# Performance work log

Hardware: AMD Instinct MI355X
Metric: run time of the kernel (lower is better)

## Reference

```python
import jax, jax.numpy as jnp
import numpy as np

FEATURES = 4096
BATCH = 2048


def setup_inputs() -> dict:
    key = jax.random.key(0)
    kx, kk = jax.random.split(key)
    x = jax.random.normal(kx, (BATCH, FEATURES), dtype=jnp.float32)
    kernel = jax.random.normal(kk, (FEATURES,), dtype=jnp.float32)
    return {"x": x, "kernel": kernel}


def reference(x, kernel):
    n = kernel.shape[0]
    i = jnp.arange(n)[:, None]   # [n,1]
    j = jnp.arange(n)[None, :]   # [1,n]
    idx = i - j                   # Toeplitz offsets
    # W[i,j] = kernel[i-j] if i>=j else 0  (causal lower-triangular Toeplitz)
    W = jnp.where(idx >= 0, kernel[jnp.clip(idx, 0, n - 1)], 0.0)
    # out[b,i] = sum_{j<=i} x[b,j] * kernel[i-j]  == x @ W.T
    return x @ W.T
```

## Files before the change

kernel.cpp:

```cpp
#include <hip/hip_runtime.h>
#include <hip/hip_bf16.h>


typedef unsigned short u16;
typedef __attribute__((ext_vector_type(8))) short  bf16x8;
typedef __attribute__((ext_vector_type(8))) unsigned short u16x8;
typedef __attribute__((ext_vector_type(4))) float  f32x4;

#define KDIM 4096
#define NDIM 4096
#define MDIM 2048
#define KREV_STRIDE 4608
#define KREV_BYTES  (8 * KREV_STRIDE * 2)
#define BSTRIDE 520

static __device__ inline u16 f2bf(float f) {
  unsigned u = __builtin_bit_cast(unsigned, f);
  unsigned r = u + 0x7FFFu + ((u >> 16) & 1u);
  return (u16)(r >> 16);
}

static __device__ inline void async_copy16(const void* g, void* l) {
  __builtin_amdgcn_global_load_lds((const __attribute__((address_space(1))) void*)g,
                                   (__attribute__((address_space(3))) void*)l,
                                   16, 0, 0);
}

__global__ __launch_bounds__(256) void prep(const float* __restrict__ x,
                                            const float* __restrict__ kern,
                                            u16* __restrict__ xb,
                                            u16* __restrict__ krevs,
                                            int conv_blocks) {
  int kb = (int)blockIdx.x - conv_blocks;
  if (kb >= 0) {
    int u = kb * 256 + threadIdx.x;
    for (int a = 0; a < 8; ++a) {
      int t = u + a - 8;
      u16 v = 0;
      if (t >= 0 && t <= 4095) v = f2bf(kern[4095 - t]);
      krevs[a * KREV_STRIDE + u] = v;
    }
  } else {
    size_t i = ((size_t)blockIdx.x * 256 + threadIdx.x) * 8;
    const f32x4* p = (const f32x4*)(x + i);
    f32x4 v0 = p[0], v1 = p[1];
    u16x8 r;
    r[0] = f2bf(v0[0]); r[1] = f2bf(v0[1]); r[2] = f2bf(v0[2]); r[3] = f2bf(v0[3]);
    r[4] = f2bf(v1[0]); r[5] = f2bf(v1[1]); r[6] = f2bf(v1[2]); r[7] = f2bf(v1[3]);
    *(u16x8*)(xb + i) = r;
  }
}

template <bool CONV>
__global__ __launch_bounds__(256, 3) void toeplitz_gemm(const void* __restrict__ Av,
                                                        const u16* __restrict__ krevs,
                                                        float* __restrict__ out) {
  __shared__ u16 A_lds[2][128 * 64];
  __shared__ u16 B_lds[2][8 * BSTRIDE];

  const int tid  = threadIdx.x;
  const int w    = tid >> 6;
  const int lane = tid & 63;
  const int lane16 = lane & 15;
  const int quad   = lane >> 4;
  const int wm = w >> 1;
  const int wn = w & 1;

  const int b    = (int)blockIdx.x;
  const int rank = (b < 256) ? b : 511 - (b & 255);
  const int ct   = 31 - (rank >> 4);
  const int n0   = ct * 128;
  const int m0   = (rank & 15) * 128;
  const int W    = 3968 - n0;

  int boff[4];
  for (int fn = 0; fn < 4; ++fn) {
    int n_g = n0 + wn * 64 + fn * 16 + lane16;
    int s0  = 4095 - n_g + quad * 8;
    int a   = s0 & 7;
    int ub  = s0 - a + 8 - W;
    boff[fn] = a * BSTRIDE + ub;
  }

  f32x4 acc[4][4] = {};
  const int nk = 2 * ct + 2;

  const int srow8 = lane >> 3;
  const int ssrc  = ((lane & 7) ^ srow8) * 8;

  const u16* xb = (const u16*)Av;
  const float* xf = (const float*)Av;

  auto stageA = [&](int ks) {
    const int buf = ks & 1;
    const int k0  = ks * 64;
    if constexpr (CONV) {
      int row  = tid & 127;
      int colq = tid >> 7;
      for (int lc = 0; lc < 4; ++lc) {
        int l = colq * 4 + lc;
        int p = l ^ (row & 7);
        const f32x4* px = (const f32x4*)(xf + (size_t)(m0 + row) * KDIM + k0 + l * 8);
        f32x4 v0 = px[0], v1 = px[1];
        u16x8 r;
        r[0]=f2bf(v0[0]); r[1]=f2bf(v0[1]); r[2]=f2bf(v0[2]); r[3]=f2bf(v0[3]);
        r[4]=f2bf(v1[0]); r[5]=f2bf(v1[1]); r[6]=f2bf(v1[2]); r[7]=f2bf(v1[3]);
        *(u16x8*)(&A_lds[buf][row * 64 + p * 8]) = r;
      }
    } else {
      for (int c = 0; c < 4; ++c) {
        int g   = c * 4 + w;
        int row = g * 8 + srow8;
        async_copy16(xb + (size_t)(m0 + row) * KDIM + k0 + ssrc,
                     &A_lds[buf][g * 512]);
      }
    }
  };
  auto stageB = [&](int ch) {
    const int bb = ch & 1;
    for (int cc = 0; cc < 2; ++cc) {
      int c = cc * 4 + w;
      async_copy16(krevs + c * KREV_STRIDE + W + ch * 256 + (lane << 3),
                   &B_lds[bb][c * BSTRIDE]);
    }
  };

  stageB(0);
  stageA(0);

  for (int ks = 0; ks < nk; ++ks) {
    __syncthreads();
    const int nxt = ks + 1;
    if (nxt < nk) {
      stageA(nxt);
      if ((nxt & 3) == 0) stageB(nxt >> 2);
    }
    const u16* Ab = A_lds[ks & 1];
    const u16* Bb = B_lds[(ks >> 2) & 1];
    const int ksl = (ks & 3) * 64;
    for (int kk = 0; kk < 2; ++kk) {
      bf16x8 af[4];
      const int p = (kk * 4 + quad) ^ (lane16 & 7);
      for (int fm = 0; fm < 4; ++fm) {
        int row = wm * 64 + fm * 16 + lane16;
        af[fm] = *(const bf16x8*)(&Ab[row * 64 + p * 8]);
      }
      bf16x8 bf[4];
      for (int fn = 0; fn < 4; ++fn)
        bf[fn] = *(const bf16x8*)(&Bb[boff[fn] + ksl + kk * 32]);
      for (int fm = 0; fm < 4; ++fm)
        for (int fn = 0; fn < 4; ++fn)
          acc[fm][fn] = __builtin_amdgcn_mfma_f32_16x16x32_bf16(af[fm], bf[fn], acc[fm][fn], 0, 0, 0);
    }
  }

  for (int fm = 0; fm < 4; ++fm) {
    int row_base = m0 + wm * 64 + fm * 16 + quad * 4;
    for (int fn = 0; fn < 4; ++fn) {
      int col = n0 + wn * 64 + fn * 16 + lane16;
      for (int r = 0; r < 4; ++r)
        out[(size_t)(row_base + r) * NDIM + col] = acc[fm][fn][r];
    }
  }
}

extern "C" void kernel_launch(void* const* d_in, const int* in_sizes, int n_in,
                              void* d_out, int out_size, void* d_ws, size_t ws_size,
                              hipStream_t stream) {
  const float* x    = (const float*)d_in[0];
  const float* kern = (const float*)d_in[1];
  float* out = (float*)d_out;

  u16* krevs = (u16*)d_ws;
  u16* xb    = (u16*)((char*)d_ws + KREV_BYTES);
  const size_t need_fast = (size_t)KREV_BYTES + (size_t)MDIM * KDIM * 2;

  if (ws_size >= need_fast) {
    prep<<<4096 + 18, 256, 0, stream>>>(x, kern, xb, krevs, 4096);
    toeplitz_gemm<false><<<512, 256, 0, stream>>>(xb, krevs, out);
  } else {
    prep<<<18, 256, 0, stream>>>(x, kern, xb, krevs, 0);
    toeplitz_gemm<true><<<512, 256, 0, stream>>>(x, krevs, out);
  }
}
```

Before: 135.9 us.

## Split K across two wave groups per block with LDS reduction

Doubles the block to 512 threads and splits each 128-wide K step between two groups of four waves. Each group accumulates its own half, and the partials are combined through shared memory before group 0 writes the output. Double buffering of A is replaced by one buffer per group, with two barriers per iteration. The goal is more waves in flight per tile to hide latency. The cost is extra synchronisation, more register pressure at 512 threads, and the reduction epilogue.

New measurement: 125.9 us. 7.3% less time.

```diff
diff --git a/kernel.cpp b/kernel.cpp
--- a/kernel.cpp
+++ b/kernel.cpp
@@ -52,19 +52,23 @@
 }
 
 template <bool CONV>
-__global__ __launch_bounds__(256, 3) void toeplitz_gemm(const void* __restrict__ Av,
+__global__ __launch_bounds__(512, 4) void toeplitz_gemm(const void* __restrict__ Av,
                                                         const u16* __restrict__ krevs,
                                                         float* __restrict__ out) {
-  __shared__ u16 A_lds[2][128 * 64];
-  __shared__ u16 B_lds[2][8 * BSTRIDE];
+  __shared__ __align__(16) char smem_raw[49408];
+  u16*   A_all = (u16*)smem_raw;
+  u16*   B_all = (u16*)(smem_raw + 32768);
+  f32x4* ep    = (f32x4*)smem_raw;
 
   const int tid  = threadIdx.x;
   const int w    = tid >> 6;
+  const int g    = w >> 2;
+  const int wl   = w & 3;
   const int lane = tid & 63;
   const int lane16 = lane & 15;
   const int quad   = lane >> 4;
-  const int wm = w >> 1;
-  const int wn = w & 1;
+  const int wm = wl >> 1;
+  const int wn = wl & 1;
 
   const int b    = (int)blockIdx.x;
   const int rank = (b < 256) ? b : 511 - (b & 255);
@@ -78,72 +82,61 @@
     int n_g = n0 + wn * 64 + fn * 16 + lane16;
     int s0  = 4095 - n_g + quad * 8;
     int a   = s0 & 7;
-    int ub  = s0 - a + 8 - W;
-    boff[fn] = a * BSTRIDE + ub;
+    boff[fn] = a * BSTRIDE + (s0 - a + 8 - W);
   }
 
   f32x4 acc[4][4] = {};
-  const int nk = 2 * ct + 2;
-
   const int srow8 = lane >> 3;
   const int ssrc  = ((lane & 7) ^ srow8) * 8;
 
-  const u16* xb = (const u16*)Av;
+  const u16*  xb = (const u16*)Av;
   const float* xf = (const float*)Av;
-
-  auto stageA = [&](int ks) {
-    const int buf = ks & 1;
-    const int k0  = ks * 64;
+  u16* A_g = A_all + g * 8192;
+
+  auto stageA = [&](int t) {
+    const int k0 = t * 128 + g * 64;
     if constexpr (CONV) {
-      int row  = tid & 127;
-      int colq = tid >> 7;
+      int j    = tid & 255;
+      int row  = j >> 1;
+      int lh   = j & 1;
       for (int lc = 0; lc < 4; ++lc) {
-        int l = colq * 4 + lc;
+        int l = lh * 4 + lc;
         int p = l ^ (row & 7);
         const f32x4* px = (const f32x4*)(xf + (size_t)(m0 + row) * KDIM + k0 + l * 8);
         f32x4 v0 = px[0], v1 = px[1];
         u16x8 r;
         r[0]=f2bf(v0[0]); r[1]=f2bf(v0[1]); r[2]=f2bf(v0[2]); r[3]=f2bf(v0[3]);
         r[4]=f2bf(v1[0]); r[5]=f2bf(v1[1]); r[6]=f2bf(v1[2]); r[7]=f2bf(v1[3]);
-        *(u16x8*)(&A_lds[buf][row * 64 + p * 8]) = r;
+        *(u16x8*)(&A_g[row * 64 + p * 8]) = r;
       }
     } else {
       for (int c = 0; c < 4; ++c) {
-        int g   = c * 4 + w;
-        int row = g * 8 + srow8;
+        int g8  = c * 4 + wl;
+        int row = g8 * 8 + srow8;
         async_copy16(xb + (size_t)(m0 + row) * KDIM + k0 + ssrc,
-                     &A_lds[buf][g * 512]);
+                     &A_g[g8 * 512]);
       }
     }
   };
-  auto stageB = [&](int ch) {
-    const int bb = ch & 1;
-    for (int cc = 0; cc < 2; ++cc) {
-      int c = cc * 4 + w;
-      async_copy16(krevs + c * KREV_STRIDE + W + ch * 256 + (lane << 3),
-                   &B_lds[bb][c * BSTRIDE]);
-    }
+  auto stageB = [&](int c) {
+    async_copy16(krevs + w * KREV_STRIDE + W + c * 256 + (lane << 3),
+                 &B_all[(c & 1) * 4160 + w * BSTRIDE]);
   };
 
   stageB(0);
   stageA(0);
 
-  for (int ks = 0; ks < nk; ++ks) {
-    __syncthreads();
-    const int nxt = ks + 1;
-    if (nxt < nk) {
-      stageA(nxt);
-      if ((nxt & 3) == 0) stageB(nxt >> 2);
-    }
-    const u16* Ab = A_lds[ks & 1];
-    const u16* Bb = B_lds[(ks >> 2) & 1];
-    const int ksl = (ks & 3) * 64;
+  const int cmax = ct >> 1;
+  for (int t = 0; ; ++t) {
+    __syncthreads();
+    const u16* Bb  = B_all + ((t >> 1) & 1) * 4160;
+    const int  ksl = (t & 1) * 128 + g * 64;
     for (int kk = 0; kk < 2; ++kk) {
       bf16x8 af[4];
       const int p = (kk * 4 + quad) ^ (lane16 & 7);
       for (int fm = 0; fm < 4; ++fm) {
         int row = wm * 64 + fm * 16 + lane16;
-        af[fm] = *(const bf16x8*)(&Ab[row * 64 + p * 8]);
+        af[fm] = *(const bf16x8*)(&A_g[row * 64 + p * 8]);
       }
       bf16x8 bf[4];
       for (int fn = 0; fn < 4; ++fn)
@@ -152,14 +145,36 @@
         for (int fn = 0; fn < 4; ++fn)
           acc[fm][fn] = __builtin_amdgcn_mfma_f32_16x16x32_bf16(af[fm], bf[fn], acc[fm][fn], 0, 0, 0);
     }
-  }
-
-  for (int fm = 0; fm < 4; ++fm) {
-    int row_base = m0 + wm * 64 + fm * 16 + quad * 4;
-    for (int fn = 0; fn < 4; ++fn) {
-      int col = n0 + wn * 64 + fn * 16 + lane16;
-      for (int r = 0; r < 4; ++r)
-        out[(size_t)(row_base + r) * NDIM + col] = acc[fm][fn][r];
+    if (t == ct) break;
+    __syncthreads();
+    stageA(t + 1);
+    if (!(t & 1) && ((t >> 1) + 1) <= cmax) stageB((t >> 1) + 1);
+  }
+
+  const int j = tid & 255;
+  for (int r = 0; r < 2; ++r) {
+    __syncthreads();
+    if (g == 1) {
+      for (int fm2 = 0; fm2 < 2; ++fm2)
+        for (int fn = 0; fn < 4; ++fn)
+          ep[j * 9 + fm2 * 4 + fn] = acc[r * 2 + fm2][fn];
+    }
+    __syncthreads();
+    if (g == 0) {
+      for (int fm2 = 0; fm2 < 2; ++fm2)
+        for (int fn = 0; fn < 4; ++fn)
+          acc[r * 2 + fm2][fn] += ep[j * 9 + fm2 * 4 + fn];
+    }
+  }
+
+  if (g == 0) {
+    for (int fm = 0; fm < 4; ++fm) {
+      int row_base = m0 + wm * 64 + fm * 16 + quad * 4;
+      for (int fn = 0; fn < 4; ++fn) {
+        int col = n0 + wn * 64 + fn * 16 + lane16;
+        for (int r = 0; r < 4; ++r)
+          out[(size_t)(row_base + r) * NDIM + col] = acc[fm][fn][r];
+      }
     }
   }
 }
@@ -177,9 +192,9 @@
 
   if (ws_size >= need_fast) {
     prep<<<4096 + 18, 256, 0, stream>>>(x, kern, xb, krevs, 4096);
-    toeplitz_gemm<false><<<512, 256, 0, stream>>>(xb, krevs, out);
+    toeplitz_gemm<false><<<512, 512, 0, stream>>>(xb, krevs, out);
   } else {
     prep<<<18, 256, 0, stream>>>(x, kern, xb, krevs, 0);
-    toeplitz_gemm<true><<<512, 256, 0, stream>>>(x, krevs, out);
-  }
-}
+    toeplitz_gemm<true><<<512, 512, 0, stream>>>(x, krevs, out);
+  }
+}
```
